# Kernel tuning notes

Hardware: AMD Instinct MI355X
Metric: run time of the kernel (lower is better)

The kernel has to match this reference:

```python
import jax, jax.numpy as jnp
import numpy as np
from jax import lax

B, CIN, COUT, H, W, K = 8, 256, 256, 64, 64, 3
KK = K * K
PAD, STRIDE = 1, 1
EPS = 1e-5


def setup_inputs() -> dict:
    key = jax.random.key(0)
    k0, k1, k2 = jax.random.split(key, 3)
    x = jax.random.normal(k0, (B, CIN, H, W), jnp.float32)
    # offset/mask predicting conv: 3*K*K output channels (o1, o2, mask)
    w_off = jax.random.normal(k1, (3 * KK, CIN, K, K), jnp.float32) * 0.01
    b_off = jnp.zeros((3 * KK,), jnp.float32)
    # main deformable conv weight
    weight = jax.random.normal(k2, (COUT, CIN, K, K), jnp.float32) / np.sqrt(CIN * KK).astype(np.float32)
    bias = jnp.zeros((COUT,), jnp.float32)
    gamma = jnp.ones((COUT,), jnp.float32)
    beta = jnp.zeros((COUT,), jnp.float32)
    return {"x": x, "w_off": w_off, "b_off": b_off, "weight": weight,
            "bias": bias, "gamma": gamma, "beta": beta}


def _bilinear_sample(img, ph, pw):
    """img: [C,H,W]; ph,pw: [KK,H,W] float sample positions. Zero outside. -> [C,KK,H,W]"""
    h0 = jnp.floor(ph).astype(jnp.int32)
    w0 = jnp.floor(pw).astype(jnp.int32)
    h1, w1 = h0 + 1, w0 + 1
    lh = ph - h0.astype(ph.dtype)
    lw = pw - w0.astype(pw.dtype)
    hh, hw = 1.0 - lh, 1.0 - lw

    def corner(hi, wi):
        valid = (hi >= 0) & (hi < H) & (wi >= 0) & (wi < W)
        hc = jnp.clip(hi, 0, H - 1)
        wc = jnp.clip(wi, 0, W - 1)
        v = img[:, hc, wc]  # [C,KK,H,W]
        return v * valid.astype(img.dtype)[None]

    return (corner(h0, w0) * (hh * hw)[None] + corner(h0, w1) * (hh * lw)[None]
            + corner(h1, w0) * (lh * hw)[None] + corner(h1, w1) * (lh * lw)[None])


def _forward(x, w_off, b_off, weight, bias, gamma, beta):
    dn = ('NCHW', 'OIHW', 'NCHW')
    # offset/mask branch (standard conv)
    om = lax.conv_general_dilated(x, w_off, (STRIDE, STRIDE), ((PAD, PAD), (PAD, PAD)),
                                  dimension_numbers=dn) + b_off[None, :, None, None]
    o1, o2, m = jnp.split(om, 3, axis=1)
    offset = jnp.concatenate([o1, o2], axis=1)          # [B, 2*KK, H, W]
    off_h = offset[:, 0::2]                             # [B, KK, H, W] dy per tap
    off_w = offset[:, 1::2]                             # [B, KK, H, W] dx per tap
    mask = jax.nn.sigmoid(m)                            # [B, KK, H, W]

    taps = jnp.arange(KK)
    base_h = (taps // K - PAD).astype(jnp.float32)[:, None, None] \
        + (jnp.arange(H, dtype=jnp.float32) * STRIDE)[None, :, None]  # [KK,H,1]
    base_w = (taps % K - PAD).astype(jnp.float32)[:, None, None] \
        + (jnp.arange(W, dtype=jnp.float32) * STRIDE)[None, None, :]  # [KK,1,W]
    ph = base_h[None] + off_h                           # [B,KK,H,W]
    pw = base_w[None] + off_w

    sampled = jax.vmap(_bilinear_sample)(x, ph, pw)     # [B,CIN,KK,H,W]
    sampled = sampled * mask[:, None]                   # modulated (DCNv2)

    y = jnp.einsum('bckhw,ock->bohw', sampled, weight.reshape(COUT, CIN, KK))
    y = y + bias[None, :, None, None]

    # BatchNorm2d (training mode: batch statistics) + ReLU
    mean = y.mean(axis=(0, 2, 3))
    var = y.var(axis=(0, 2, 3))
    yn = (y - mean[None, :, None, None]) * lax.rsqrt(var + EPS)[None, :, None, None]
    out = jax.nn.relu(gamma[None, :, None, None] * yn + beta[None, :, None, None])
    return out


def reference(x, w_off, b_off, weight, bias, gamma, beta):
    return _forward(x, w_off, b_off, weight, bias, gamma, beta)
```

## Files before the change

kernel.cpp:

```cpp
#include <hip/hip_runtime.h>
#include <cstdint>

#define BB    8
#define CIN   256
#define COUT  256
#define HH    64
#define WW    64
#define HWSZ  4096
#define NPIX  32768
#define NTAP  9

typedef __attribute__((ext_vector_type(8))) short    s16x8;
typedef __attribute__((ext_vector_type(8))) unsigned short u16x8;
typedef __attribute__((ext_vector_type(4))) unsigned short u16x4;
typedef __attribute__((ext_vector_type(4))) float    f32x4;

__device__ __forceinline__ float bf2f(unsigned short u) {
    unsigned int v = ((unsigned int)u) << 16;
    return __builtin_bit_cast(float, v);
}
__device__ __forceinline__ unsigned short f2bf(float f) {
    unsigned int u = __builtin_bit_cast(unsigned int, f);
    unsigned int r = (u + 0x7FFFu + ((u >> 16) & 1u)) >> 16;
    return (unsigned short)r;
}

__global__ void k_pack_x(const float* __restrict__ x, unsigned short* __restrict__ xT) {
    int blk = blockIdx.x;
    int b    = blk & 7;
    int rest = blk >> 3;
    int h    = rest >> 2;
    int c0   = (rest & 3) * 64;
    __shared__ float tile[64][65];
    int t = threadIdx.x;
#pragma unroll
    for (int r = 0; r < 16; ++r) {
        int idx = t + r * 256;
        int i = idx >> 6, w = idx & 63;
        tile[i][w] = x[(((b * 256 + c0 + i) * 64 + h) * 64) + w];
    }
    __syncthreads();
#pragma unroll
    for (int r = 0; r < 16; ++r) {
        int idx = t + r * 256;
        int w = idx >> 6, c = idx & 63;
        xT[((b * 64 + h) * 64 + w) * 256 + c0 + c] = f2bf(tile[c][w]);
    }
}

__global__ void k_pack_wk(const float* __restrict__ w, unsigned short* __restrict__ wT) {
    int idx = blockIdx.x * 256 + threadIdx.x;
    int j   = idx & 7;
    int q   = (idx >> 3) & 3;
    int o16 = (idx >> 5) & 15;
    int n16 = (idx >> 9) & 15;
    int kc  = (idx >> 13) & 7;
    int tp  = idx >> 16;
    int c = kc * 32 + q * 8 + j;
    int o = n16 * 16 + o16;
    wT[idx] = f2bf(w[(o * 256 + c) * 9 + tp]);
}

__global__ void k_pack_woff(const float* __restrict__ w, unsigned short* __restrict__ wT) {
    int idx = blockIdx.x * 256 + threadIdx.x;
    int c  = idx & 255;
    int j  = (idx >> 8) & 31;
    int tp = idx >> 13;
    float v = (j < 27) ? w[(j * 256 + c) * 9 + tp] : 0.f;
    wT[idx] = f2bf(v);
}

__global__ __launch_bounds__(256, 2)
void k_offconv(const unsigned short* __restrict__ xT,
               const unsigned short* __restrict__ wofT,
               const float* __restrict__ b_off,
               float* __restrict__ om) {
    int blk = blockIdx.x;
    int b = blk & 7, h = blk >> 3;
    int P0 = (b * 64 + h) * 64;
    int t = threadIdx.x;
    int lane = t & 63, wv = t >> 6;
    int p0w = wv * 16;
    int lm = lane & 15, q = lane >> 4;
    __shared__ unsigned short S3[3 * 66 * 136];

    const f32x4 FZ = {0.f, 0.f, 0.f, 0.f};
    f32x4 acc0 = FZ, acc1 = FZ;

    for (int cc = 0; cc < 2; ++cc) {
        __syncthreads();
        if (t < 96) {
            int rr = t >> 5, col = (t >> 4) & 1, c8 = (t & 15) * 8;
            u16x8 z = {0,0,0,0,0,0,0,0};
            *reinterpret_cast<u16x8*>(&S3[(rr * 66 + col * 65) * 136 + c8]) = z;
        }
#pragma unroll
        for (int r = 0; r < 12; ++r) {
            int v = t + r * 256;
            int rr = v >> 10, rem = v & 1023;
            int w = rem >> 4, c8 = (rem & 15) * 8;
            int hr = h + rr - 1;
            u16x8 d = {0,0,0,0,0,0,0,0};
            if (hr >= 0 && hr < 64)
                d = *reinterpret_cast<const u16x8*>(xT + ((b * 64 + hr) * 64 + w) * 256 + cc * 128 + c8);
            *reinterpret_cast<u16x8*>(&S3[(rr * 66 + w + 1) * 136 + c8]) = d;
        }
        __syncthreads();
#pragma unroll
        for (int tp = 0; tp < 9; ++tp) {
            int dh = tp / 3, dw = tp % 3;
            const unsigned short* wb = wofT + (tp * 32 + lm) * 256 + cc * 128;
#pragma unroll
            for (int kc = 0; kc < 4; ++kc) {
                s16x8 a = *reinterpret_cast<const s16x8*>(&S3[(dh * 66 + p0w + lm + dw) * 136 + kc * 32 + q * 8]);
                s16x8 b0 = *reinterpret_cast<const s16x8*>(wb + kc * 32 + q * 8);
                s16x8 b1 = *reinterpret_cast<const s16x8*>(wb + 16 * 256 + kc * 32 + q * 8);
                acc0 = __builtin_amdgcn_mfma_f32_16x16x32_bf16(a, b0, acc0, 0, 0, 0);
                acc1 = __builtin_amdgcn_mfma_f32_16x16x32_bf16(a, b1, acc1, 0, 0, 0);
            }
        }
    }
#pragma unroll
    for (int n = 0; n < 2; ++n) {
        int j = n * 16 + lm;
        float bj = (j < 27) ? b_off[j] : 0.f;
        f32x4 a = n ? acc1 : acc0;
#pragma unroll
        for (int i = 0; i < 4; ++i) {
            int prow = p0w + q * 4 + i;
            om[(P0 + prow) * 32 + j] = a[i] + bj;
        }
    }
}

__global__ __launch_bounds__(512, 2)
void k_main(const unsigned short* __restrict__ xT,
            const unsigned short* __restrict__ wTk,
            const float* __restrict__ om,
            const float* __restrict__ bias,
            unsigned short* __restrict__ y16,
            float* __restrict__ gsum, float* __restrict__ gssq) {
    int blk = blockIdx.x;
    int b = blk & 7, h = blk >> 3;
    int pblk = b * 64 + h;
    int P0 = pblk * 64;
    int t = threadIdx.x;
    int lane = t & 63, wv = t >> 6;
    int lm = lane & 15, q = lane >> 4;
    int o0 = wv * 32;

    __shared__ unsigned short S[2][64 * 264];
    __shared__ float OMS[64 * 32];

    {
        float4 tmp = *reinterpret_cast<const float4*>(om + P0 * 32 + t * 4);
        *reinterpret_cast<float4*>(&OMS[t * 4]) = tmp;
    }
    __syncthreads();

    const f32x4 FZ = {0.f, 0.f, 0.f, 0.f};
    f32x4 acc[4][2];
#pragma unroll
    for (int m = 0; m < 4; ++m)
#pragma unroll
        for (int n = 0; n < 2; ++n) acc[m][n] = FZ;

    int p  = wv * 8 + (lane >> 3);
    int s  = lane & 7;
    int rb = b * 4096;

    float w00, w01, w10, w11;
    int a00, a01, a10, a11;
    u16x8 r00[4], r01[4], r10[4], r11[4];

    auto setup = [&](int tp) {
        float oh = OMS[p * 32 + 2 * tp];
        float ow = OMS[p * 32 + 2 * tp + 1];
        float mv = OMS[p * 32 + 18 + tp];
        float mk = 1.f / (1.f + __expf(-mv));
        float ph = (float)(h + tp / 3 - 1) + oh;
        float pw = (float)(p + tp % 3 - 1) + ow;
        float fh0 = floorf(ph), fw0 = floorf(pw);
        int ih0 = (int)fh0, iw0 = (int)fw0;
        float lh = ph - fh0, lw = pw - fw0;
        float hh = 1.f - lh, hw_ = 1.f - lw;
        bool vh0 = (ih0 >= 0) & (ih0 < 64);
        bool vh1 = (ih0 + 1 >= 0) & (ih0 + 1 < 64);
        bool vw0 = (iw0 >= 0) & (iw0 < 64);
        bool vw1 = (iw0 + 1 >= 0) & (iw0 + 1 < 64);
        w00 = hh * hw_ * mk * (float)(vh0 & vw0);
        w01 = hh * lw  * mk * (float)(vh0 & vw1);
        w10 = lh * hw_ * mk * (float)(vh1 & vw0);
        w11 = lh * lw  * mk * (float)(vh1 & vw1);
        int ch0 = min(max(ih0, 0), 63), ch1 = min(max(ih0 + 1, 0), 63);
        int cw0 = min(max(iw0, 0), 63), cw1 = min(max(iw0 + 1, 0), 63);
        a00 = ((rb + ch0 * 64 + cw0) * 256) + s * 8;
        a01 = ((rb + ch0 * 64 + cw1) * 256) + s * 8;
        a10 = ((rb + ch1 * 64 + cw0) * 256) + s * 8;
        a11 = ((rb + ch1 * 64 + cw1) * 256) + s * 8;
    };
    auto issue = [&]() {
#pragma unroll
        for (int j = 0; j < 4; ++j) {
            r00[j] = *reinterpret_cast<const u16x8*>(xT + a00 + j * 64);
            r01[j] = *reinterpret_cast<const u16x8*>(xT + a01 + j * 64);
            r10[j] = *reinterpret_cast<const u16x8*>(xT + a10 + j * 64);
            r11[j] = *reinterpret_cast<const u16x8*>(xT + a11 + j * 64);
        }
    };

    setup(0);
    issue();

    for (int tp = 0; tp < 9; ++tp) {
        int cur = tp & 1;
#pragma unroll
        for (int j = 0; j < 4; ++j) {
            u16x8 res;
#pragma unroll
            for (int k = 0; k < 8; ++k) {
                float v = w00 * bf2f(r00[j][k]);
                v = fmaf(w01, bf2f(r01[j][k]), v);
                v = fmaf(w10, bf2f(r10[j][k]), v);
                v = fmaf(w11, bf2f(r11[j][k]), v);
                res[k] = f2bf(v);
            }
            *reinterpret_cast<u16x8*>(&S[cur][p * 264 + j * 64 + s * 8]) = res;
        }
        __syncthreads();

        if (tp < 8) {
            setup(tp + 1);
            issue();
        }

        const unsigned short* wtap = wTk + (size_t)tp * 65536 + (size_t)(wv * 2) * 512
                                   + lm * 32 + q * 8;
#pragma unroll
        for (int kc = 0; kc < 8; ++kc) {
            const unsigned short* wb = wtap + kc * 8192;
            s16x8 b0 = *reinterpret_cast<const s16x8*>(wb);
            s16x8 b1 = *reinterpret_cast<const s16x8*>(wb + 512);
#pragma unroll
            for (int mt = 0; mt < 4; ++mt) {
                s16x8 a = *reinterpret_cast<const s16x8*>(&S[cur][(mt * 16 + lm) * 264 + kc * 32 + q * 8]);
                acc[mt][0] = __builtin_amdgcn_mfma_f32_16x16x32_bf16(a, b0, acc[mt][0], 0, 0, 0);
                acc[mt][1] = __builtin_amdgcn_mfma_f32_16x16x32_bf16(a, b1, acc[mt][1], 0, 0, 0);
            }
        }
    }

    u16x4* yv = reinterpret_cast<u16x4*>(y16);
#pragma unroll
    for (int nt = 0; nt < 2; ++nt) {
        int o = o0 + nt * 16 + lm;
        float bo = bias[o];
        float sacc = 0.f, ssacc = 0.f;
#pragma unroll
        for (int mt = 0; mt < 4; ++mt) {
            u16x4 st;
#pragma unroll
            for (int i = 0; i < 4; ++i) {
                float v = acc[mt][nt][i] + bo;
                st[i] = f2bf(v);
                sacc += v; ssacc += v * v;
            }
            int idx4 = (((pblk * 8 + wv) * 2 + nt) * 4 + mt) * 64 + lane;
            yv[idx4] = st;
        }
        sacc  += __shfl_xor(sacc, 16);
        sacc  += __shfl_xor(sacc, 32);
        ssacc += __shfl_xor(ssacc, 16);
        ssacc += __shfl_xor(ssacc, 32);
        if (q == 0) {
            atomicAdd(&gsum[o], sacc);
            atomicAdd(&gssq[o], ssacc);
        }
    }
}

__global__ void k_bnrelu(const unsigned short* __restrict__ y16,
                         const float* __restrict__ gsum, const float* __restrict__ gssq,
                         const float* __restrict__ gamma, const float* __restrict__ beta,
                         float* __restrict__ out) {
    int blk = blockIdx.x;
    int b = blk & 7, h = blk >> 3;
    int pblk = b * 64 + h;
    __shared__ unsigned short T[64 * 257];
    __shared__ float sc[256], sh[256];
    int t = threadIdx.x;
    {
        const float n = 32768.f;
        float mean = gsum[t] / n;
        float var = gssq[t] / n - mean * mean;
        float inv = rsqrtf(var + 1e-5f);
        float s = gamma[t] * inv;
        sc[t] = s;
        sh[t] = beta[t] - mean * s;
    }
    const u16x4* yv = reinterpret_cast<const u16x4*>(y16) + pblk * 4096;
#pragma unroll
    for (int r = 0; r < 16; ++r) {
        int v = t + r * 256;
        u16x4 d = yv[v];
        int lane = v & 63, mt = (v >> 6) & 3, nt = (v >> 8) & 1, wvv = (v >> 9) & 7;
        int p = mt * 16 + (lane >> 4) * 4;
        int o = wvv * 32 + nt * 16 + (lane & 15);
        T[(p + 0) * 257 + o] = d[0];
        T[(p + 1) * 257 + o] = d[1];
        T[(p + 2) * 257 + o] = d[2];
        T[(p + 3) * 257 + o] = d[3];
    }
    __syncthreads();
    int w = t & 63;
    int ob = (t >> 6) * 64;
    float* obase = out + (size_t)b * (256 * 4096) + h * 64 + w;
#pragma unroll 4
    for (int rr = 0; rr < 64; ++rr) {
        int o = ob + rr;
        float v = bf2f(T[w * 257 + o]);
        obase[(size_t)o * 4096] = fmaxf(v * sc[o] + sh[o], 0.f);
    }
}

extern "C" void kernel_launch(void* const* d_in, const int* in_sizes, int n_in,
                              void* d_out, int out_size, void* d_ws, size_t ws_size,
                              hipStream_t stream) {
    const float* x      = (const float*)d_in[0];
    const float* w_off  = (const float*)d_in[1];
    const float* b_off  = (const float*)d_in[2];
    const float* weight = (const float*)d_in[3];
    const float* bias   = (const float*)d_in[4];
    const float* gamma  = (const float*)d_in[5];
    const float* beta   = (const float*)d_in[6];

    char* ws = (char*)d_ws;
    const size_t OFF_XT    = 0;
    const size_t OFF_WT    = OFF_XT + 16777216;
    const size_t OFF_WOFT  = OFF_WT + 1179648;
    const size_t OFF_OM    = OFF_WOFT + 147456;
    const size_t OFF_Y16   = OFF_OM + 4194304;
    const size_t OFF_SUM   = OFF_Y16 + 16777216;
    const size_t OFF_SUMSQ = OFF_SUM + 1024;

    unsigned short* xT   = (unsigned short*)(ws + OFF_XT);
    unsigned short* wTk  = (unsigned short*)(ws + OFF_WT);
    unsigned short* wofT = (unsigned short*)(ws + OFF_WOFT);
    float* om    = (float*)(ws + OFF_OM);
    unsigned short* y16  = (unsigned short*)(ws + OFF_Y16);
    float* sum   = (float*)(ws + OFF_SUM);
    float* sumsq = (float*)(ws + OFF_SUMSQ);

    hipMemsetAsync(ws + OFF_SUM, 0, 2048, stream);

    k_pack_x   <<<2048, 256, 0, stream>>>(x, xT);
    k_pack_wk  <<<2304, 256, 0, stream>>>(weight, wTk);
    k_pack_woff<<< 288, 256, 0, stream>>>(w_off, wofT);
    k_offconv  <<< 512, 256, 0, stream>>>(xT, wofT, b_off, om);
    k_main     <<< 512, 512, 0, stream>>>(xT, wTk, om, bias, y16, sum, sumsq);
    k_bnrelu   <<< 512, 256, 0, stream>>>(y16, sum, sumsq, gamma, beta, (float*)d_out);
}
```

Baseline: 227.1 us.

## Warp-specialize k_main into gather producer waves and MFMA consumer waves

Splits the 8 waves of k_main into 4 producer waves that do the bilinear gather and blend into the shared-memory double buffer, and 4 consumer waves that run the MFMA GEMM over 64 output channels each. Tap fills and matrix work are meant to overlap across the two groups, replacing the old scheme where every wave did both in sequence. The bnrelu index decode is updated for the new y16 tile layout, and launch bounds are raised to ask for more resident blocks. In exchange, only half the waves issue MFMAs, the consumers hold twice as many accumulators, and the higher occupancy target may force register spills.

New measurement: 216.7 us. 4.6% less time.

```diff
diff --git a/kernel.cpp b/kernel.cpp
--- a/kernel.cpp
+++ b/kernel.cpp
@@ -133,7 +133,7 @@
     }
 }
 
-__global__ __launch_bounds__(512, 2)
+__global__ __launch_bounds__(512, 4)
 void k_main(const unsigned short* __restrict__ xT,
             const unsigned short* __restrict__ wTk,
             const float* __restrict__ om,
@@ -147,10 +147,9 @@
     int t = threadIdx.x;
     int lane = t & 63, wv = t >> 6;
     int lm = lane & 15, q = lane >> 4;
-    int o0 = wv * 32;
 
     __shared__ unsigned short S[2][64 * 264];
-    __shared__ float OMS[64 * 32];
+    __shared__ float OMS[2048];
 
     {
         float4 tmp = *reinterpret_cast<const float4*>(om + P0 * 32 + t * 4);
@@ -158,123 +157,145 @@
     }
     __syncthreads();
 
-    const f32x4 FZ = {0.f, 0.f, 0.f, 0.f};
-    f32x4 acc[4][2];
-#pragma unroll
-    for (int m = 0; m < 4; ++m)
-#pragma unroll
-        for (int n = 0; n < 2; ++n) acc[m][n] = FZ;
-
-    int p  = wv * 8 + (lane >> 3);
-    int s  = lane & 7;
-    int rb = b * 4096;
-
-    float w00, w01, w10, w11;
-    int a00, a01, a10, a11;
-    u16x8 r00[4], r01[4], r10[4], r11[4];
-
-    auto setup = [&](int tp) {
-        float oh = OMS[p * 32 + 2 * tp];
-        float ow = OMS[p * 32 + 2 * tp + 1];
-        float mv = OMS[p * 32 + 18 + tp];
-        float mk = 1.f / (1.f + __expf(-mv));
-        float ph = (float)(h + tp / 3 - 1) + oh;
-        float pw = (float)(p + tp % 3 - 1) + ow;
-        float fh0 = floorf(ph), fw0 = floorf(pw);
-        int ih0 = (int)fh0, iw0 = (int)fw0;
-        float lh = ph - fh0, lw = pw - fw0;
-        float hh = 1.f - lh, hw_ = 1.f - lw;
-        bool vh0 = (ih0 >= 0) & (ih0 < 64);
-        bool vh1 = (ih0 + 1 >= 0) & (ih0 + 1 < 64);
-        bool vw0 = (iw0 >= 0) & (iw0 < 64);
-        bool vw1 = (iw0 + 1 >= 0) & (iw0 + 1 < 64);
-        w00 = hh * hw_ * mk * (float)(vh0 & vw0);
-        w01 = hh * lw  * mk * (float)(vh0 & vw1);
-        w10 = lh * hw_ * mk * (float)(vh1 & vw0);
-        w11 = lh * lw  * mk * (float)(vh1 & vw1);
-        int ch0 = min(max(ih0, 0), 63), ch1 = min(max(ih0 + 1, 0), 63);
-        int cw0 = min(max(iw0, 0), 63), cw1 = min(max(iw0 + 1, 0), 63);
-        a00 = ((rb + ch0 * 64 + cw0) * 256) + s * 8;
-        a01 = ((rb + ch0 * 64 + cw1) * 256) + s * 8;
-        a10 = ((rb + ch1 * 64 + cw0) * 256) + s * 8;
-        a11 = ((rb + ch1 * 64 + cw1) * 256) + s * 8;
-    };
-    auto issue = [&]() {
-#pragma unroll
-        for (int j = 0; j < 4; ++j) {
-            r00[j] = *reinterpret_cast<const u16x8*>(xT + a00 + j * 64);
-            r01[j] = *reinterpret_cast<const u16x8*>(xT + a01 + j * 64);
-            r10[j] = *reinterpret_cast<const u16x8*>(xT + a10 + j * 64);
-            r11[j] = *reinterpret_cast<const u16x8*>(xT + a11 + j * 64);
-        }
-    };
-
-    setup(0);
-    issue();
-
-    for (int tp = 0; tp < 9; ++tp) {
-        int cur = tp & 1;
-#pragma unroll
-        for (int j = 0; j < 4; ++j) {
-            u16x8 res;
-#pragma unroll
-            for (int k = 0; k < 8; ++k) {
-                float v = w00 * bf2f(r00[j][k]);
-                v = fmaf(w01, bf2f(r01[j][k]), v);
-                v = fmaf(w10, bf2f(r10[j][k]), v);
-                v = fmaf(w11, bf2f(r11[j][k]), v);
-                res[k] = f2bf(v);
-            }
-            *reinterpret_cast<u16x8*>(&S[cur][p * 264 + j * 64 + s * 8]) = res;
-        }
+    if (wv >= 4) {
+        int pw = wv - 4;
+        int p  = pw * 16 + (lane >> 2);
+        int s2 = lane & 3;
+        int rb = b * 4096;
+        float w00, w01, w10, w11;
+        int a00, a01, a10, a11;
+
+        auto setup = [&](int tp) {
+            float oh = OMS[p * 32 + 2 * tp];
+            float ow = OMS[p * 32 + 2 * tp + 1];
+            float mv = OMS[p * 32 + 18 + tp];
+            float mk = 1.f / (1.f + __expf(-mv));
+            float ph = (float)(h + tp / 3 - 1) + oh;
+            float pw_ = (float)(p + tp % 3 - 1) + ow;
+            float fh0 = floorf(ph), fw0 = floorf(pw_);
+            int ih0 = (int)fh0, iw0 = (int)fw0;
+            float lh = ph - fh0, lw = pw_ - fw0;
+            float hh = 1.f - lh, hw_ = 1.f - lw;
+            bool vh0 = (ih0 >= 0) & (ih0 < 64);
+            bool vh1 = (ih0 + 1 >= 0) & (ih0 + 1 < 64);
+            bool vw0 = (iw0 >= 0) & (iw0 < 64);
+            bool vw1 = (iw0 + 1 >= 0) & (iw0 + 1 < 64);
+            w00 = hh * hw_ * mk * (float)(vh0 & vw0);
+            w01 = hh * lw  * mk * (float)(vh0 & vw1);
+            w10 = lh * hw_ * mk * (float)(vh1 & vw0);
+            w11 = lh * lw  * mk * (float)(vh1 & vw1);
+            int ch0 = min(max(ih0, 0), 63), ch1 = min(max(ih0 + 1, 0), 63);
+            int cw0 = min(max(iw0, 0), 63), cw1 = min(max(iw0 + 1, 0), 63);
+            a00 = ((rb + ch0 * 64 + cw0) * 256) + s2 * 8;
+            a01 = ((rb + ch0 * 64 + cw1) * 256) + s2 * 8;
+            a10 = ((rb + ch1 * 64 + cw0) * 256) + s2 * 8;
+            a11 = ((rb + ch1 * 64 + cw1) * 256) + s2 * 8;
+        };
+
+        u16x8 rA[8], rB[8];
+        auto issueQ = [&](int qq, u16x8* r) {
+            int co = qq * 64;
+#pragma unroll
+            for (int j = 0; j < 2; ++j) {
+                r[0 + j] = *reinterpret_cast<const u16x8*>(xT + a00 + co + j * 32);
+                r[2 + j] = *reinterpret_cast<const u16x8*>(xT + a01 + co + j * 32);
+                r[4 + j] = *reinterpret_cast<const u16x8*>(xT + a10 + co + j * 32);
+                r[6 + j] = *reinterpret_cast<const u16x8*>(xT + a11 + co + j * 32);
+            }
+        };
+        auto blendQ = [&](int buf, int qq, u16x8* r) {
+#pragma unroll
+            for (int j = 0; j < 2; ++j) {
+                u16x8 res;
+#pragma unroll
+                for (int k = 0; k < 8; ++k) {
+                    float v = w00 * bf2f(r[0 + j][k]);
+                    v = fmaf(w01, bf2f(r[2 + j][k]), v);
+                    v = fmaf(w10, bf2f(r[4 + j][k]), v);
+                    v = fmaf(w11, bf2f(r[6 + j][k]), v);
+                    res[k] = f2bf(v);
+                }
+                *reinterpret_cast<u16x8*>(&S[buf][p * 264 + qq * 64 + j * 32 + s2 * 8]) = res;
+            }
+        };
+        auto fillTap = [&](int tp, int buf) {
+            setup(tp);
+            issueQ(0, rA);
+            issueQ(1, rB);
+            blendQ(buf, 0, rA);
+            issueQ(2, rA);
+            blendQ(buf, 1, rB);
+            issueQ(3, rB);
+            blendQ(buf, 2, rA);
+            blendQ(buf, 3, rB);
+        };
+
+        fillTap(0, 0);
         __syncthreads();
-
-        if (tp < 8) {
-            setup(tp + 1);
-            issue();
-        }
-
-        const unsigned short* wtap = wTk + (size_t)tp * 65536 + (size_t)(wv * 2) * 512
-                                   + lm * 32 + q * 8;
-#pragma unroll
-        for (int kc = 0; kc < 8; ++kc) {
-            const unsigned short* wb = wtap + kc * 8192;
-            s16x8 b0 = *reinterpret_cast<const s16x8*>(wb);
-            s16x8 b1 = *reinterpret_cast<const s16x8*>(wb + 512);
+        for (int tp = 0; tp < 9; ++tp) {
+            if (tp < 8) fillTap(tp + 1, (tp + 1) & 1);
+            __syncthreads();
+        }
+    } else {
+        int o0 = wv * 64;
+        const f32x4 FZ = {0.f, 0.f, 0.f, 0.f};
+        f32x4 acc[4][4];
+#pragma unroll
+        for (int m = 0; m < 4; ++m)
+#pragma unroll
+            for (int n = 0; n < 4; ++n) acc[m][n] = FZ;
+
+        __syncthreads();
+        for (int tp = 0; tp < 9; ++tp) {
+            const unsigned short* Sc = &S[tp & 1][0];
+            const unsigned short* wtap = wTk + (size_t)tp * 65536
+                                       + (size_t)(wv * 4) * 512 + lm * 32 + q * 8;
+#pragma unroll
+            for (int kc = 0; kc < 8; ++kc) {
+                const unsigned short* wb = wtap + kc * 8192;
+                s16x8 bf0 = *reinterpret_cast<const s16x8*>(wb);
+                s16x8 bf1 = *reinterpret_cast<const s16x8*>(wb + 512);
+                s16x8 bf2 = *reinterpret_cast<const s16x8*>(wb + 1024);
+                s16x8 bf3 = *reinterpret_cast<const s16x8*>(wb + 1536);
+#pragma unroll
+                for (int mt = 0; mt < 4; ++mt) {
+                    s16x8 a = *reinterpret_cast<const s16x8*>(
+                        &Sc[(mt * 16 + lm) * 264 + kc * 32 + q * 8]);
+                    acc[mt][0] = __builtin_amdgcn_mfma_f32_16x16x32_bf16(a, bf0, acc[mt][0], 0, 0, 0);
+                    acc[mt][1] = __builtin_amdgcn_mfma_f32_16x16x32_bf16(a, bf1, acc[mt][1], 0, 0, 0);
+                    acc[mt][2] = __builtin_amdgcn_mfma_f32_16x16x32_bf16(a, bf2, acc[mt][2], 0, 0, 0);
+                    acc[mt][3] = __builtin_amdgcn_mfma_f32_16x16x32_bf16(a, bf3, acc[mt][3], 0, 0, 0);
+                }
+            }
+            __syncthreads();
+        }
+
+        u16x4* yv = reinterpret_cast<u16x4*>(y16);
+#pragma unroll
+        for (int nt = 0; nt < 4; ++nt) {
+            int o = o0 + nt * 16 + lm;
+            float bo = bias[o];
+            float sacc = 0.f, ssacc = 0.f;
 #pragma unroll
             for (int mt = 0; mt < 4; ++mt) {
-                s16x8 a = *reinterpret_cast<const s16x8*>(&S[cur][(mt * 16 + lm) * 264 + kc * 32 + q * 8]);
-                acc[mt][0] = __builtin_amdgcn_mfma_f32_16x16x32_bf16(a, b0, acc[mt][0], 0, 0, 0);
-                acc[mt][1] = __builtin_amdgcn_mfma_f32_16x16x32_bf16(a, b1, acc[mt][1], 0, 0, 0);
-            }
-        }
-    }
-
-    u16x4* yv = reinterpret_cast<u16x4*>(y16);
-#pragma unroll
-    for (int nt = 0; nt < 2; ++nt) {
-        int o = o0 + nt * 16 + lm;
-        float bo = bias[o];
-        float sacc = 0.f, ssacc = 0.f;
-#pragma unroll
-        for (int mt = 0; mt < 4; ++mt) {
-            u16x4 st;
-#pragma unroll
-            for (int i = 0; i < 4; ++i) {
-                float v = acc[mt][nt][i] + bo;
-                st[i] = f2bf(v);
-                sacc += v; ssacc += v * v;
-            }
-            int idx4 = (((pblk * 8 + wv) * 2 + nt) * 4 + mt) * 64 + lane;
-            yv[idx4] = st;
-        }
-        sacc  += __shfl_xor(sacc, 16);
-        sacc  += __shfl_xor(sacc, 32);
-        ssacc += __shfl_xor(ssacc, 16);
-        ssacc += __shfl_xor(ssacc, 32);
-        if (q == 0) {
-            atomicAdd(&gsum[o], sacc);
-            atomicAdd(&gssq[o], ssacc);
+                u16x4 st;
+#pragma unroll
+                for (int i = 0; i < 4; ++i) {
+                    float v = acc[mt][nt][i] + bo;
+                    st[i] = f2bf(v);
+                    sacc += v; ssacc += v * v;
+                }
+                int idx4 = ((pblk * 4 + wv) * 16 + nt * 4 + mt) * 64 + lane;
+                yv[idx4] = st;
+            }
+            sacc  += __shfl_xor(sacc, 16);
+            sacc  += __shfl_xor(sacc, 32);
+            ssacc += __shfl_xor(ssacc, 16);
+            ssacc += __shfl_xor(ssacc, 32);
+            if (q == 0) {
+                atomicAdd(&gsum[o], sacc);
+                atomicAdd(&gssq[o], ssacc);
+            }
         }
     }
 }
@@ -303,9 +324,9 @@
     for (int r = 0; r < 16; ++r) {
         int v = t + r * 256;
         u16x4 d = yv[v];
-        int lane = v & 63, mt = (v >> 6) & 3, nt = (v >> 8) & 1, wvv = (v >> 9) & 7;
+        int lane = v & 63, mt = (v >> 6) & 3, nt = (v >> 8) & 3, wvv = (v >> 10) & 3;
         int p = mt * 16 + (lane >> 4) * 4;
-        int o = wvv * 32 + nt * 16 + (lane & 15);
+        int o = wvv * 64 + nt * 16 + (lane & 15);
         T[(p + 0) * 257 + o] = d[0];
         T[(p + 1) * 257 + o] = d[1];
         T[(p + 2) * 257 + o] = d[2];
```
